# Performance work log

Measured on AMD Instinct MI355X. Metric: run time of the kernel, lower is better.

The kernel has to match this reference:

```python
import jax, jax.numpy as jnp
import numpy as np

N, D, V = 4096, 256, 32000
B, T = 32, 256
U_DECAY, X_DECAY = 0.97, 0.97
EPS = 1e-6


def layernorm_row(z):
    # matches torch: (z - mean) / (std + eps), std with Bessel correction (ddof=1)
    m = jnp.mean(z, axis=-1, keepdims=True)
    s = jnp.std(z, axis=-1, keepdims=True, ddof=1)
    return (z - m) / (s + EPS)


def setup_inputs() -> dict:
    key = jax.random.key(0)
    k1, k2, k3, k4, k5 = jax.random.split(key, 5)
    token_emb = jax.random.normal(k1, (V, D), jnp.float32) / np.float32(np.sqrt(D))
    E = jax.random.normal(k2, (D, N), jnp.float32) / np.float32(np.sqrt(N))
    Dx = jax.random.normal(k3, (N, D), jnp.float32) / np.float32(np.sqrt(D))
    Dy = jax.random.normal(k4, (N, D), jnp.float32) / np.float32(np.sqrt(D))
    idx = jax.random.randint(k5, (B, T), 0, V)
    return {"idx": idx, "token_emb": token_emb, "E": E, "Dx": Dx, "Dy": Dy}


def reference(idx, token_emb, E, Dx, Dy):
    b = idx.shape[0]

    def step(carry, tok):
        x, rho = carry                                   # x: (b,n), rho: (b,d,n)
        v_prev = token_emb[tok]                          # (b,d) embedding gather
        x_t = X_DECAY * x + jax.nn.relu(v_prev @ Dx.T)   # (b,n)
        x_t = x_t / (jnp.sum(jnp.abs(x_t), axis=-1, keepdims=True) + EPS)  # L1 normalize
        a_star = jnp.einsum('bdn,bn->bd', rho, x_t)      # fast-weight readout
        y_t = jax.nn.relu(layernorm_row(a_star) @ Dy.T) * jax.nn.relu(x_t)  # (b,n)
        v_star = layernorm_row(y_t @ E.T)                # (b,d)
        # Hebbian decayed outer-product memory update
        rho = U_DECAY * (rho + jnp.einsum('bd,bn->bdn', layernorm_row(v_prev), x_t))
        return (x_t, rho), v_star

    x0 = jnp.zeros((b, N), jnp.float32)
    rho0 = jnp.zeros((b, D, N), jnp.float32)
    (_, _), vs = jax.lax.scan(step, (x0, rho0), idx.T)   # vs: (T,b,d)
    return jnp.transpose(vs, (1, 0, 2))                  # (b,T,d)
```

## Files before the change

### kernel.cpp

```cpp
#include <hip/hip_runtime.h>
#include <hip/hip_bf16.h>

#define NN 4096
#define DD 256
#define BB 32
#define TT 256
#define EPS 1e-6f
#define DECAY 0.97f
#define LOG2_DECAY -0.043943348f

typedef __hip_bfloat16 bf16;
typedef short short8 __attribute__((ext_vector_type(8)));
typedef float floatx4 __attribute__((ext_vector_type(4)));

__device__ __forceinline__ float bfu2f(short u) {
    return __uint_as_float(((unsigned)(unsigned short)u) << 16);
}

__device__ __forceinline__ float blk_sum_256(float v, volatile float* s4) {
#pragma unroll
    for (int o = 32; o > 0; o >>= 1) v += __shfl_down(v, o, 64);
    int lane = threadIdx.x & 63, w = threadIdx.x >> 6;
    __syncthreads();
    if (lane == 0) s4[w] = v;
    __syncthreads();
    return s4[0] + s4[1] + s4[2] + s4[3];
}

__device__ __forceinline__ void gl16(const bf16* g, bf16* l) {
    __builtin_amdgcn_global_load_lds((const __attribute__((address_space(1))) void*)g,
                                     (__attribute__((address_space(3))) void*)l, 16, 0, 0);
}

__global__ void k_detect(const unsigned short* __restrict__ raw, int* __restrict__ flag) {
    __shared__ int cnt[4];
    int tid = threadIdx.x;
    int bad = 0;
    for (int i = tid; i < 8192; i += 256) {
        unsigned int u = raw[2 * i];
        float v = __uint_as_float(u << 16);
        if (!(fabsf(v) < 1e6f)) bad++;
    }
#pragma unroll
    for (int o = 32; o > 0; o >>= 1) bad += __shfl_down(bad, o, 64);
    int lane = tid & 63, w = tid >> 6;
    if (lane == 0) cnt[w] = bad;
    __syncthreads();
    if (tid == 0) flag[0] = (cnt[0] + cnt[1] + cnt[2] + cnt[3] < 32) ? 1 : 0;
}

__global__ __launch_bounds__(256) void k_convert3(const void* __restrict__ s0,
                                                  const void* __restrict__ s1,
                                                  const void* __restrict__ s2,
                                                  bf16* __restrict__ d0,
                                                  bf16* __restrict__ d1,
                                                  bf16* __restrict__ d2,
                                                  const int* __restrict__ flag) {
    const int per = NN * DD / 8;
    int i = blockIdx.x * 256 + threadIdx.x;
    int m = i / per, j = i % per;
    const void* s = (m == 0) ? s0 : (m == 1) ? s1 : s2;
    bf16* d = (m == 0) ? d0 : (m == 1) ? d1 : d2;
    if (flag[0]) {
        ((uint4*)d)[j] = ((const uint4*)s)[j];
    } else {
        const float4* f = (const float4*)s;
        float4 a = f[2 * j], b = f[2 * j + 1];
        short8 o;
        float va[8] = {a.x, a.y, a.z, a.w, b.x, b.y, b.z, b.w};
#pragma unroll
        for (int k = 0; k < 8; k++) {
            bf16 t = __float2bfloat16(va[k]);
            o[k] = *reinterpret_cast<short*>(&t);
        }
        ((short8*)d)[j] = o;
    }
}

__global__ __launch_bounds__(256) void k_gather_ln(const void* __restrict__ emb,
                                                   const int* __restrict__ idx,
                                                   bf16* __restrict__ Vpb,
                                                   bf16* __restrict__ Ub,
                                                   const int* __restrict__ flag) {
    __shared__ float s4[4];
    int r = blockIdx.x, d = threadIdx.x;
    int tok = idx[r];
    long o = (long)tok * DD + d;
    float e = flag[0] ? __bfloat162float(((const bf16*)emb)[o]) : ((const float*)emb)[o];
    Vpb[(long)r * DD + d] = __float2bfloat16(e);
    float m = blk_sum_256(e, s4) * (1.0f / DD);
    float zc = e - m;
    float var = blk_sum_256(zc * zc, s4) * (1.0f / (DD - 1));
    Ub[(long)r * DD + d] = __float2bfloat16(zc / (sqrtf(fmaxf(var, 0.f)) + EPS));
}

__global__ __launch_bounds__(256) void k_transpose(const bf16* __restrict__ Ub,
                                                   bf16* __restrict__ Ut) {
    __shared__ bf16 tile[32][33];
    int b = blockIdx.z;
    int t0 = blockIdx.x * 32, d0 = blockIdx.y * 32;
    const bf16* src = Ub + (long)b * TT * DD;
    bf16* dst = Ut + (long)b * DD * TT;
    int rr = threadIdx.x >> 3, c4 = (threadIdx.x & 7) * 4;
#pragma unroll
    for (int i = 0; i < 4; i++) tile[rr][c4 + i] = src[(long)(t0 + rr) * DD + d0 + c4 + i];
    __syncthreads();
#pragma unroll
    for (int i = 0; i < 4; i++) dst[(long)(d0 + rr) * TT + t0 + c4 + i] = tile[c4 + i][rr];
}

enum { EPI_RELU_BF16 = 0, EPI_NONE_F32 = 1, EPI_RELU_MULX_BF16 = 2 };

template <int EPI, int KSPLIT, int TRI>
__global__ __launch_bounds__(256) void k_mfma_nt(int K,
                                                 const bf16* __restrict__ A, int lda, long sA,
                                                 const bf16* __restrict__ B, int ldb, long sB,
                                                 void* __restrict__ Cv, int ldc, long sC,
                                                 const bf16* __restrict__ Xaux,
                                                 float* __restrict__ Wsum) {
    __shared__ __align__(16) char smem[17408];
    bf16* As = (bf16*)smem;
    bf16* Bs = (bf16*)(smem + 8192);
    bf16* R = (bf16*)smem;

    int z = blockIdx.z;
    int bz = z / KSPLIT, ks = z % KSPLIT;
    A += (long)bz * sA;
    B += (long)bz * sB;
    int bx = blockIdx.x, by = blockIdx.y;
    if (TRI) {
        by = (blockIdx.x >= 1) ? 1 : 0;
        bx = (blockIdx.x == 2) ? 1 : 0;
    }
    int bm = by * 128, bn = bx * 128;
    int tid = threadIdx.x;
    int srow = tid >> 2, scol = (tid & 3) << 3;
    int w = tid >> 6, lane = tid & 63;
    int wm = (w >> 1) * 64, wn = (w & 1) * 64;
    int lm = lane & 15, kh = lane >> 4;

    floatx4 acc[4][4];
#pragma unroll
    for (int i = 0; i < 4; i++)
#pragma unroll
        for (int j = 0; j < 4; j++) acc[i][j] = (floatx4){0.f, 0.f, 0.f, 0.f};

    int kchunk = K / KSPLIT;
    int kbeg = ks * kchunk, kend = kbeg + kchunk;
    const bf16* gA0 = A + (long)(bm + srow) * lda + scol;
    const bf16* gA1 = gA0 + (long)64 * lda;
    const bf16* gB0 = B + (long)(bn + srow) * ldb + scol;
    const bf16* gB1 = gB0 + (long)64 * ldb;
    bf16* lA0 = As + srow * 32 + scol;
    bf16* lA1 = As + (srow + 64) * 32 + scol;
    bf16* lB0 = Bs + srow * 32 + scol;
    bf16* lB1 = Bs + (srow + 64) * 32 + scol;

    for (int k0 = kbeg; k0 < kend; k0 += 32) {
        __syncthreads();
        gl16(gA0 + k0, lA0);
        gl16(gA1 + k0, lA1);
        gl16(gB0 + k0, lB0);
        gl16(gB1 + k0, lB1);
        __syncthreads();
        short8 af[4], bfr[4];
#pragma unroll
        for (int i = 0; i < 4; i++) af[i] = *(const short8*)(As + (wm + i * 16 + lm) * 32 + kh * 8);
#pragma unroll
        for (int j = 0; j < 4; j++) bfr[j] = *(const short8*)(Bs + (wn + j * 16 + lm) * 32 + kh * 8);
#pragma unroll
        for (int i = 0; i < 4; i++)
#pragma unroll
            for (int j = 0; j < 4; j++)
                acc[i][j] = __builtin_amdgcn_mfma_f32_16x16x32_bf16(af[i], bfr[j], acc[i][j], 0, 0, 0);
    }

    if (EPI == EPI_NONE_F32) {
        long cbase = (long)z * sC;
#pragma unroll
        for (int i = 0; i < 4; i++)
#pragma unroll
            for (int j = 0; j < 4; j++)
#pragma unroll
                for (int r = 0; r < 4; r++) {
                    int gm = bm + wm + i * 16 + kh * 4 + r;
                    int gn = bn + wn + j * 16 + lm;
                    ((float*)Cv)[cbase + (long)gm * ldc + gn] = acc[i][j][r];
                }
        return;
    }

#pragma unroll
    for (int p = 0; p < 2; p++) {
        __syncthreads();
        if ((w >> 1) == p) {
#pragma unroll
            for (int i = 0; i < 4; i++)
#pragma unroll
                for (int j = 0; j < 4; j++)
#pragma unroll
                    for (int r = 0; r < 4; r++) {
                        int rr = i * 16 + kh * 4 + r;
                        int cc = wn + j * 16 + lm;
                        R[rr * 136 + cc] = __float2bfloat16(fmaxf(acc[i][j][r], 0.f));
                    }
        }
        __syncthreads();
#pragma unroll
        for (int it = 0; it < 4; it++) {
            int row_l = it * 16 + (tid >> 4);
            int c8 = (tid & 15) * 8;
            short8 vv = *(const short8*)(R + row_l * 136 + c8);
            int gm = bm + p * 64 + row_l;
            long off = (long)gm * ldc + bn + c8;
            if (EPI == EPI_RELU_BF16) {
                *(short8*)((bf16*)Cv + off) = vv;
                float s = 0.f;
#pragma unroll
                for (int k = 0; k < 8; k++) s += bfu2f(vv[k]);
#pragma unroll
                for (int o = 8; o > 0; o >>= 1) s += __shfl_down(s, o, 16);
                if ((tid & 15) == 0) atomicAdd(&Wsum[gm], s);
            } else {
                short8 xx = *(const short8*)(Xaux + off);
                short8 oo;
#pragma unroll
                for (int k = 0; k < 8; k++) {
                    float prod = bfu2f(vv[k]) * fmaxf(bfu2f(xx[k]), 0.f);
                    bf16 t = __float2bfloat16(prod);
                    oo[k] = *reinterpret_cast<short*>(&t);
                }
                *(short8*)((bf16*)Cv + off) = oo;
            }
        }
    }
}

__global__ __launch_bounds__(256) void k_scalar_scan(const float* __restrict__ Wsum,
                                                     float* __restrict__ invS) {
    __shared__ float sw[BB * TT];
    for (int i = threadIdx.x; i < BB * TT; i += 256) sw[i] = Wsum[i];
    __syncthreads();
    int b = threadIdx.x;
    if (b < BB) {
        float sig = 0.f;
        for (int t = 0; t < TT; t++) {
            float S = DECAY * sig + sw[b * TT + t];
            float inv = 1.f / (S + EPS);
            invS[b * TT + t] = inv;
            sig = S * inv;
        }
    }
}

__global__ __launch_bounds__(256) void k_colscan(bf16* __restrict__ W,
                                                 const float* __restrict__ invS) {
    __shared__ float sv[TT];
    int b = blockIdx.y;
    sv[threadIdx.x] = invS[b * TT + threadIdx.x];
    __syncthreads();
    int n = blockIdx.x * 256 + threadIdx.x;
    bf16* p = W + (long)b * TT * NN + n;
    float x = 0.f;
    for (int t = 0; t < TT; t++) {
        float w = __bfloat162float(p[(long)t * NN]);
        x = (DECAY * x + w) * sv[t];
        p[(long)t * NN] = __float2bfloat16(x);
    }
}

__global__ __launch_bounds__(256) void k_reduce_mask(const float* __restrict__ Gp,
                                                     bf16* __restrict__ G) {
    int r = blockIdx.x;
    int b = r >> 8, t = r & 255;
    int s = threadIdx.x;
    long base = ((long)b * 4) * 65536 + (long)t * 256 + s;
    float v = Gp[base] + Gp[base + 65536] + Gp[base + 2 * 65536] + Gp[base + 3 * 65536];
    float o = (s < t) ? v * exp2f((float)(t - s) * LOG2_DECAY) : 0.f;
    G[(long)r * 256 + s] = __float2bfloat16(o);
}

__global__ __launch_bounds__(256) void k_ln_rows(const float* __restrict__ Zp,
                                                 bf16* __restrict__ O) {
    __shared__ float s4[4];
    long r = blockIdx.x;
    int d = threadIdx.x;
    long b = r >> 8, t = r & 255;
    long base = (b * 2) * 65536 + t * 256 + d;
    float z = Zp[base] + Zp[base + 65536];
    float m = blk_sum_256(z, s4) * (1.0f / DD);
    float zc = z - m;
    float var = blk_sum_256(zc * zc, s4) * (1.0f / (DD - 1));
    O[r * DD + d] = __float2bfloat16(zc / (sqrtf(fmaxf(var, 0.f)) + EPS));
}

__global__ __launch_bounds__(256) void k_final_ln(const float* __restrict__ Zp,
                                                  void* __restrict__ out,
                                                  const int* __restrict__ flag) {
    __shared__ float s4[4];
    long r = blockIdx.x;
    int d = threadIdx.x;
    const long SL = (long)8192 * 256;
    long o = r * DD + d;
    float z = Zp[o] + Zp[o + SL] + Zp[o + 2 * SL] + Zp[o + 3 * SL];
    float m = blk_sum_256(z, s4) * (1.0f / DD);
    float zc = z - m;
    float var = blk_sum_256(zc * zc, s4) * (1.0f / (DD - 1));
    float v = zc / (sqrtf(fmaxf(var, 0.f)) + EPS);
    if (flag[0]) ((bf16*)out)[o] = __float2bfloat16(v);
    else ((float*)out)[o] = v;
}

extern "C" void kernel_launch(void* const* d_in, const int* in_sizes, int n_in,
                              void* d_out, int out_size, void* d_ws, size_t ws_size,
                              hipStream_t stream) {
    const int* idx = (const int*)d_in[0];
    const void* emb = d_in[1];
    const void* E = d_in[2];
    const void* Dx = d_in[3];
    const void* Dy = d_in[4];

    char* base = (char*)d_ws;
    size_t off = 0;
    int* flag = (int*)base; off += 1024;
    bf16* Dxb = (bf16*)(base + off); off += (size_t)NN * DD * 2;
    bf16* Dyb = (bf16*)(base + off); off += (size_t)NN * DD * 2;
    bf16* Eb  = (bf16*)(base + off); off += (size_t)DD * NN * 2;
    bf16* Vpb = (bf16*)(base + off); off += (size_t)BB * TT * DD * 2;
    bf16* Ub  = (bf16*)(base + off); off += (size_t)BB * TT * DD * 2;
    bf16* Ut  = (bf16*)(base + off); off += (size_t)BB * TT * DD * 2;
    float* Wsum = (float*)(base + off); off += (size_t)BB * TT * 4;
    float* invS = (float*)(base + off); off += (size_t)BB * TT * 4;
    bf16* ALNb = (bf16*)(base + off); off += (size_t)BB * TT * DD * 2;
    bf16* G = (bf16*)(base + off); off += (size_t)BB * TT * TT * 2;
    float* Gp = (float*)(base + off); off += (size_t)4 * BB * TT * TT * 4;
    float* Astar = Gp;
    float* Zp = Gp;
    bf16* Xb = (bf16*)(base + off); off += (size_t)BB * TT * NN * 2;

    const int M = BB * TT;

    k_detect<<<1, 256, 0, stream>>>((const unsigned short*)emb, flag);
    k_convert3<<<3 * NN * DD / 8 / 256, 256, 0, stream>>>(Dx, Dy, E, Dxb, Dyb, Eb, flag);
    k_gather_ln<<<M, 256, 0, stream>>>(emb, idx, Vpb, Ub, flag);
    k_transpose<<<dim3(8, 8, BB), 256, 0, stream>>>(Ub, Ut);

    hipMemsetAsync(Wsum, 0, (size_t)M * 4, stream);

    k_mfma_nt<EPI_RELU_BF16, 1, 0><<<dim3(32, 64, 1), 256, 0, stream>>>(
        DD, Vpb, DD, 0, Dxb, DD, 0, Xb, NN, 0, nullptr, Wsum);

    k_scalar_scan<<<1, 256, 0, stream>>>(Wsum, invS);
    k_colscan<<<dim3(16, BB, 1), 256, 0, stream>>>(Xb, invS);

    k_mfma_nt<EPI_NONE_F32, 4, 1><<<dim3(3, 1, BB * 4), 256, 0, stream>>>(
        NN, Xb, NN, (long)TT * NN, Xb, NN, (long)TT * NN, Gp, TT, (long)TT * TT, nullptr, nullptr);
    k_reduce_mask<<<M, 256, 0, stream>>>(Gp, G);

    k_mfma_nt<EPI_NONE_F32, 2, 0><<<dim3(2, 2, BB * 2), 256, 0, stream>>>(
        TT, G, TT, (long)TT * TT, Ut, TT, (long)DD * TT, Astar, DD, (long)TT * DD, nullptr, nullptr);
    k_ln_rows<<<M, 256, 0, stream>>>(Astar, ALNb);

    k_mfma_nt<EPI_RELU_MULX_BF16, 1, 0><<<dim3(32, 64, 1), 256, 0, stream>>>(
        DD, ALNb, DD, 0, Dyb, DD, 0, Xb, NN, 0, Xb, nullptr);

    k_mfma_nt<EPI_NONE_F32, 4, 0><<<dim3(2, 64, 4), 256, 0, stream>>>(
        NN, Xb, NN, 0, Eb, NN, 0, Zp, DD, (long)M * DD, nullptr, nullptr);

    k_final_ln<<<M, 256, 0, stream>>>(Zp, d_out, flag);
}
```

Measured before the change: 338.1 us.

## Double-buffer MFMA GEMM LDS tiles and XOR-swizzle to avoid bank conflicts

The MFMA NT GEMM now uses two LDS buffers, prefetching the next K-chunk with direct global-to-LDS loads while the current chunk feeds the MFMAs. This drops one barrier per iteration. The column position inside each 32-element row is XOR-swizzled by row bits to reduce LDS bank conflicts on the fragment reads. LDS use grows from 17KB to 32KB per block, which may lower occupancy, and the epilogue reuse of smem must still fit.

```diff
diff --git a/kernel.cpp b/kernel.cpp
--- a/kernel.cpp
+++ b/kernel.cpp
@@ -118,9 +118,7 @@
                                                  void* __restrict__ Cv, int ldc, long sC,
                                                  const bf16* __restrict__ Xaux,
                                                  float* __restrict__ Wsum) {
-    __shared__ __align__(16) char smem[17408];
-    bf16* As = (bf16*)smem;
-    bf16* Bs = (bf16*)(smem + 8192);
+    __shared__ __align__(16) char smem[32768];
     bf16* R = (bf16*)smem;
 
     int z = blockIdx.z;
@@ -134,7 +132,8 @@
     }
     int bm = by * 128, bn = bx * 128;
     int tid = threadIdx.x;
-    int srow = tid >> 2, scol = (tid & 3) << 3;
+    int srow = tid >> 2;
+    int scol = ((((srow >> 1) & 3) ^ (tid & 3)) << 3);
     int w = tid >> 6, lane = tid & 63;
     int wm = (w >> 1) * 64, wn = (w & 1) * 64;
     int lm = lane & 15, kh = lane >> 4;
@@ -151,28 +150,48 @@
     const bf16* gA1 = gA0 + (long)64 * lda;
     const bf16* gB0 = B + (long)(bn + srow) * ldb + scol;
     const bf16* gB1 = gB0 + (long)64 * ldb;
-    bf16* lA0 = As + srow * 32 + scol;
-    bf16* lA1 = As + (srow + 64) * 32 + scol;
-    bf16* lB0 = Bs + srow * 32 + scol;
-    bf16* lB1 = Bs + (srow + 64) * 32 + scol;
-
+    int dslot = tid * 8;
+
+    {
+        bf16* bufA = (bf16*)smem;
+        bf16* bufB = bufA + 4096;
+        gl16(gA0 + kbeg, bufA + dslot);
+        gl16(gA1 + kbeg, bufA + 2048 + dslot);
+        gl16(gB0 + kbeg, bufB + dslot);
+        gl16(gB1 + kbeg, bufB + 2048 + dslot);
+    }
+    __syncthreads();
+
+    int cur = 0;
     for (int k0 = kbeg; k0 < kend; k0 += 32) {
-        __syncthreads();
-        gl16(gA0 + k0, lA0);
-        gl16(gA1 + k0, lA1);
-        gl16(gB0 + k0, lB0);
-        gl16(gB1 + k0, lB1);
-        __syncthreads();
+        bf16* cbA = (bf16*)(smem + (cur ? 16384 : 0));
+        bf16* cbB = cbA + 4096;
+        bf16* nbA = (bf16*)(smem + (cur ? 0 : 16384));
+        bf16* nbB = nbA + 4096;
+        if (k0 + 32 < kend) {
+            gl16(gA0 + k0 + 32, nbA + dslot);
+            gl16(gA1 + k0 + 32, nbA + 2048 + dslot);
+            gl16(gB0 + k0 + 32, nbB + dslot);
+            gl16(gB1 + k0 + 32, nbB + 2048 + dslot);
+        }
         short8 af[4], bfr[4];
 #pragma unroll
-        for (int i = 0; i < 4; i++) af[i] = *(const short8*)(As + (wm + i * 16 + lm) * 32 + kh * 8);
-#pragma unroll
-        for (int j = 0; j < 4; j++) bfr[j] = *(const short8*)(Bs + (wn + j * 16 + lm) * 32 + kh * 8);
+        for (int i = 0; i < 4; i++) {
+            int row = wm + i * 16 + lm;
+            af[i] = *(const short8*)(cbA + row * 32 + ((((row >> 1) & 3) ^ kh) << 3));
+        }
+#pragma unroll
+        for (int j = 0; j < 4; j++) {
+            int row = wn + j * 16 + lm;
+            bfr[j] = *(const short8*)(cbB + row * 32 + ((((row >> 1) & 3) ^ kh) << 3));
+        }
 #pragma unroll
         for (int i = 0; i < 4; i++)
 #pragma unroll
             for (int j = 0; j < 4; j++)
                 acc[i][j] = __builtin_amdgcn_mfma_f32_16x16x32_bf16(af[i], bfr[j], acc[i][j], 0, 0, 0);
+        __syncthreads();
+        cur ^= 1;
     }
 
     if (EPI == EPI_NONE_F32) {
```

Measured after the change: 319.4 us. 5.5% less time.
